# Optimization experiments

Measured on AMD Instinct MI355X. Metric: run time of the kernel, lower is better.

Reference implementation:

```python
import jax, jax.numpy as jnp
import numpy as np

B, T, V, H, L = 2048, 128, 256, 20, 15  # batch, seq_len, vocab, hidden, max_label


def setup_inputs() -> dict:
    key = jax.random.key(0)
    ks = jax.random.split(key, 8)
    g = lambda k, shape, s: (jax.random.normal(k, shape, jnp.float32) * s)
    return {
        "x": jax.random.randint(ks[0], (B, T), 0, V, dtype=jnp.int32),
        "W0": g(ks[1], (V, 3 * H), 0.06),   # input kernel layer 0 [V, 3H] (z|r|h)
        "U0": g(ks[2], (H, 3 * H), 0.2),    # recurrent kernel layer 0
        "b0i": jnp.zeros((3 * H,), jnp.float32),  # input bias (reset_after=True split bias)
        "b0r": jnp.zeros((3 * H,), jnp.float32),  # recurrent bias
        "W1": g(ks[3], (H, 3 * H), 0.2),
        "U1": g(ks[4], (H, 3 * H), 0.2),
        "b1i": jnp.zeros((3 * H,), jnp.float32),
        "b1r": jnp.zeros((3 * H,), jnp.float32),
        "Wd": g(ks[5], (H, L), 0.2),
        "bd": jnp.zeros((L,), jnp.float32),
        "drop_rate": 0,  # identity dropout (deterministic reference)
    }


def _gru_cell(h, xw, U, br):
    # Keras GRUCell with reset_after=True:
    #   xw = x @ W + b_in  (precomputed), rec = h @ U + b_rec
    rec = h @ U + br
    xz, xr, xh = jnp.split(xw, 3, axis=-1)
    rz, rr, rh = jnp.split(rec, 3, axis=-1)
    z = jax.nn.sigmoid(xz + rz)
    r = jax.nn.sigmoid(xr + rr)
    hh = jnp.tanh(xh + r * rh)
    return z * h + (1.0 - z) * hh


def reference(x, W0, U0, b0i, b0r, W1, U1, b1i, b1r, Wd, bd, drop_rate):
    # one_hot(x) @ W0 == gather rows of W0 (same math, no [B,T,V] materialization)
    xW0 = W0[x] + b0i                 # [B, T, 3H]
    xW0 = jnp.swapaxes(xW0, 0, 1)     # [T, B, 3H] for scan over time

    def step(carry, xw_t):
        h0, h1 = carry
        h0 = _gru_cell(h0, xw_t, U0, b0r)
        xw1 = h0 @ W1 + b1i
        h1 = _gru_cell(h1, xw1, U1, b1r)
        return (h0, h1), None

    h0 = jnp.zeros((x.shape[0], H), W0.dtype)
    h1 = jnp.zeros((x.shape[0], H), W0.dtype)
    (h0, h1), _ = jax.lax.scan(step, (h0, h1), xW0)
    # tf.nn.dropout with rate 0 is the identity
    out = h1
    logits = jax.nn.softmax(out @ Wd + bd, axis=-1)  # [B, L]
    return logits
```

## Files before the change

kernel.cpp:

```cpp
#include <hip/hip_runtime.h>


#define BB 2048
#define TT 128
#define HH 20
#define LL 15
#define H3 60

typedef float v2f __attribute__((ext_vector_type(2)));

#if __has_builtin(__builtin_amdgcn_exp2f)
#define EXP2(x) __builtin_amdgcn_exp2f(x)
#else
#define EXP2(x) exp2f(x)
#endif

__device__ __forceinline__ float bclane(float v, int k) {
    return __int_as_float(__builtin_amdgcn_readlane(__float_as_int(v), k));
}
__device__ __forceinline__ float dpp_rshr1(float v) {
    return __int_as_float(__builtin_amdgcn_update_dpp(
        0, __float_as_int(v), 0x111, 0xF, 0xF, true));
}
__device__ __forceinline__ float dpp_rshr2(float v) {
    return __int_as_float(__builtin_amdgcn_update_dpp(
        0, __float_as_int(v), 0x112, 0xF, 0xF, true));
}
__device__ __forceinline__ float fast_rcp(float x) { return __builtin_amdgcn_rcpf(x); }
#define PIN(v) asm volatile("" : "+v"(v))
#define LDSFENCE() asm volatile("" ::: "memory")

extern "C" __global__ __launch_bounds__(256)
__attribute__((amdgpu_waves_per_eu(2, 2)))
void gru2_kernel(const int* __restrict__ x, const float* __restrict__ W0,
                 const float* __restrict__ U0, const float* __restrict__ b0i,
                 const float* __restrict__ b0r, const float* __restrict__ W1,
                 const float* __restrict__ U1, const float* __restrict__ b1i,
                 const float* __restrict__ b1r, const float* __restrict__ Wd,
                 const float* __restrict__ bd, float* __restrict__ out)
{
    const int lane = threadIdx.x & 63;
    const int w = threadIdx.x >> 6;
    const int b = blockIdx.x * 4 + w;
    const int row = lane >> 4;
    const int pos = lane & 15;
    const int pc  = (pos < 15) ? pos : 14;
    const int u   = pc / 3;
    const int p3  = pc % 3;
    const int j   = row * 5 + u;
    const bool home = (pos < 15) && (p3 == 2);
    const int col = p3 * 20 + j;

    const float gsc = (p3 == 2) ? -2.8853900817779268f : -1.4426950408889634f;

    __shared__ __align__(16) float hbuf[4][2][24];
    float* h0buf = &hbuf[w][0][0];
    float* h1buf = &hbuf[w][1][0];
    const float4* h0q = (const float4*)h0buf;
    const float4* h1q = (const float4*)h1buf;
    if (home) { h0buf[j] = 0.f; h1buf[j] = 0.f; }
    LDSFENCE();

    v2f u0p[10], w1p[10], u1p[10];
#pragma unroll
    for (int q = 0; q < 10; ++q) {
        const int k0 = (2 * q) * H3, k1 = (2 * q + 1) * H3;
        u0p[q] = v2f{U0[k0 + col] * gsc, U0[k1 + col] * gsc};
        w1p[q] = v2f{W1[k0 + col] * gsc, W1[k1 + col] * gsc};
        u1p[q] = v2f{U1[k0 + col] * gsc, U1[k1 + col] * gsc};
    }
#pragma unroll
    for (int q = 0; q < 10; ++q) { PIN(u0p[q]); PIN(w1p[q]); PIN(u1p[q]); }
    float bi0 = b0i[col] * gsc, br0 = b0r[col] * gsc;
    float bi1 = b1i[col] * gsc, br1 = b1r[col] * gsc;
    PIN(bi0); PIN(br0); PIN(bi1); PIN(br1);

    const int* xrow = x + b * TT;
    const int tokA = xrow[lane];
    const int tokB = xrow[64 + lane];

    float h0 = 0.f, h1 = 0.f;

    const int tok0 = __builtin_amdgcn_readlane(tokA, 0);
    const int tok1 = __builtin_amdgcn_readlane(tokA, 1);
    int tokn2 = __builtin_amdgcn_readlane(tokA, 2);
    float xw_cur = fmaf(W0[tok0 * H3 + col], gsc, bi0);
    float xw_nxt = W0[tok1 * H3 + col];

    float4 c0[5], c1[5];
    float rec0, xw1, rec1;

#define DOT01()                                                               \
    {                                                                         \
        v2f a0a = v2f{br0, 0.f}, a0b = v2f{0.f, 0.f};                         \
        v2f a1a = v2f{bi1, 0.f}, a1b = v2f{0.f, 0.f};                         \
        _Pragma("unroll")                                                     \
        for (int q = 0; q < 5; ++q) {                                         \
            const v2f hA = v2f{c0[q].x, c0[q].y}, hB = v2f{c0[q].z, c0[q].w}; \
            a0a = __builtin_elementwise_fma(hA, u0p[2 * q], a0a);             \
            a0b = __builtin_elementwise_fma(hB, u0p[2 * q + 1], a0b);         \
            a1a = __builtin_elementwise_fma(hA, w1p[2 * q], a1a);             \
            a1b = __builtin_elementwise_fma(hB, w1p[2 * q + 1], a1b);         \
        }                                                                     \
        { const v2f t = a0a + a0b; rec0 = t.x + t.y; }                        \
        { const v2f t = a1a + a1b; xw1  = t.x + t.y; }                        \
    }
#define DOT2()                                                                \
    {                                                                         \
        v2f a2a = v2f{br1, 0.f}, a2b = v2f{0.f, 0.f};                         \
        _Pragma("unroll")                                                     \
        for (int q = 0; q < 5; ++q) {                                         \
            const v2f gA = v2f{c1[q].x, c1[q].y}, gB = v2f{c1[q].z, c1[q].w}; \
            a2a = __builtin_elementwise_fma(gA, u1p[2 * q], a2a);             \
            a2b = __builtin_elementwise_fma(gB, u1p[2 * q + 1], a2b);         \
        }                                                                     \
        { const v2f t = a2a + a2b; rec1 = t.x + t.y; }                        \
    }
#define GATES(XW, REC, H)                                                     \
    {                                                                         \
        const float e  = EXP2((XW) + (REC));                                  \
        const float t  = fast_rcp(1.f + e);                                   \
        const float rv = dpp_rshr1(t);                                        \
        const float zv = dpp_rshr2(t);                                        \
        const float eh = EXP2(fmaf(rv, (REC), (XW)));                         \
        const float th = fast_rcp(1.f + eh);                                  \
        const float hh = fmaf(2.f, th, -1.f);                                 \
        H = fmaf(zv, (H) - hh, hh);                                           \
    }

    {
        const float pf = W0[tokn2 * H3 + col];
        const int tokn3 = __builtin_amdgcn_readlane(tokA, 3);
        GATES(xw_cur, br0, h0);
        if (home) h0buf[j] = h0;
        LDSFENCE();
#pragma unroll
        for (int q = 0; q < 5; ++q) { c0[q] = h0q[q]; c1[q] = h1q[q]; }
        xw_cur = fmaf(xw_nxt, gsc, bi0); xw_nxt = pf; tokn2 = tokn3;
        DOT01();
    }

#pragma unroll 2
    for (int i = 1; i < TT; ++i) {
        const int t3 = (i + 3 < TT) ? (i + 3) : (TT - 1);
        const float pf = W0[tokn2 * H3 + col];
        const int tokn3 = __builtin_amdgcn_readlane(t3 < 64 ? tokA : tokB, t3 & 63);

        GATES(xw_cur, rec0, h0);
        if (home) h0buf[j] = h0;
        LDSFENCE();
#pragma unroll
        for (int q = 0; q < 5; ++q) c0[q] = h0q[q];

        DOT2();

        GATES(xw1, rec1, h1);
        if (home) h1buf[j] = h1;
        LDSFENCE();
#pragma unroll
        for (int q = 0; q < 5; ++q) c1[q] = h1q[q];

        xw_cur = fmaf(xw_nxt, gsc, bi0); xw_nxt = pf; tokn2 = tokn3;

        DOT01();
    }

    {
        DOT2();
        GATES(xw1, rec1, h1);
        if (home) h1buf[j] = h1;
        LDSFENCE();
    }

    const int l = lane < LL ? lane : LL - 1;
    float acc = bd[l];
#pragma unroll
    for (int k = 0; k < HH; ++k)
        acc = fmaf(h1buf[k], Wd[k * LL + l], acc);

    float m = acc;
#pragma unroll
    for (int i = 0; i < LL; ++i) m = fmaxf(m, bclane(acc, i));
    const float e = __expf(acc - m);
    float s = 0.f;
#pragma unroll
    for (int i = 0; i < LL; ++i) s += bclane(e, i);
    const float pr = e * fast_rcp(s);

    if (lane < LL) out[b * LL + lane] = pr;
}

extern "C" void kernel_launch(void* const* d_in, const int* in_sizes, int n_in,
                              void* d_out, int out_size, void* d_ws, size_t ws_size,
                              hipStream_t stream) {
    const int*   x   = (const int*)  d_in[0];
    const float* W0  = (const float*)d_in[1];
    const float* U0  = (const float*)d_in[2];
    const float* b0i = (const float*)d_in[3];
    const float* b0r = (const float*)d_in[4];
    const float* W1  = (const float*)d_in[5];
    const float* U1  = (const float*)d_in[6];
    const float* b1i = (const float*)d_in[7];
    const float* b1r = (const float*)d_in[8];
    const float* Wd  = (const float*)d_in[9];
    const float* bd  = (const float*)d_in[10];
    float* out = (float*)d_out;

    dim3 grid(BB / 4), block(256);
    hipLaunchKernelGGL(gru2_kernel, grid, block, 0, stream,
                       x, W0, U0, b0i, b0r, W1, U1, b1i, b1r, Wd, bd, out);
}
```

Measured before the change: 121.2 us.

## Process two batch sequences per wave to interleave independent recurrences

Each wave now runs two batch rows at once, interleaving their GRU recurrences so the latency of one chain's gate math, DPP shuffles and LDS round-trips can be hidden behind the other's work. The grid is halved to 256 blocks and the waves-per-EU hint drops from 2 to 1 to leave room for the doubled register state. This trades thread-level parallelism for instruction-level parallelism. With 256 blocks of 4 waves the whole problem is 1024 waves, so it depends on the per-wave ILP hiding latency that occupancy used to cover.

```diff
diff --git a/kernel.cpp b/kernel.cpp
--- a/kernel.cpp
+++ b/kernel.cpp
@@ -31,7 +31,7 @@
 #define LDSFENCE() asm volatile("" ::: "memory")
 
 extern "C" __global__ __launch_bounds__(256)
-__attribute__((amdgpu_waves_per_eu(2, 2)))
+__attribute__((amdgpu_waves_per_eu(1, 1)))
 void gru2_kernel(const int* __restrict__ x, const float* __restrict__ W0,
                  const float* __restrict__ U0, const float* __restrict__ b0i,
                  const float* __restrict__ b0r, const float* __restrict__ W1,
@@ -41,7 +41,6 @@
 {
     const int lane = threadIdx.x & 63;
     const int w = threadIdx.x >> 6;
-    const int b = blockIdx.x * 4 + w;
     const int row = lane >> 4;
     const int pos = lane & 15;
     const int pc  = (pos < 15) ? pos : 14;
@@ -53,12 +52,16 @@
 
     const float gsc = (p3 == 2) ? -2.8853900817779268f : -1.4426950408889634f;
 
-    __shared__ __align__(16) float hbuf[4][2][24];
-    float* h0buf = &hbuf[w][0][0];
-    float* h1buf = &hbuf[w][1][0];
-    const float4* h0q = (const float4*)h0buf;
-    const float4* h1q = (const float4*)h1buf;
-    if (home) { h0buf[j] = 0.f; h1buf[j] = 0.f; }
+    __shared__ __align__(16) float hbuf[4][2][2][24];
+    float* hA0 = &hbuf[w][0][0][0];
+    float* hA1 = &hbuf[w][0][1][0];
+    float* hB0 = &hbuf[w][1][0][0];
+    float* hB1 = &hbuf[w][1][1][0];
+    const float4* qA0 = (const float4*)hA0;
+    const float4* qA1 = (const float4*)hA1;
+    const float4* qB0 = (const float4*)hB0;
+    const float4* qB1 = (const float4*)hB1;
+    if (home) { hA0[j] = 0.f; hA1[j] = 0.f; hB0[j] = 0.f; hB1[j] = 0.f; }
     LDSFENCE();
 
     v2f u0p[10], w1p[10], u1p[10];
@@ -75,119 +78,153 @@
     float bi1 = b1i[col] * gsc, br1 = b1r[col] * gsc;
     PIN(bi0); PIN(br0); PIN(bi1); PIN(br1);
 
-    const int* xrow = x + b * TT;
-    const int tokA = xrow[lane];
-    const int tokB = xrow[64 + lane];
-
-    float h0 = 0.f, h1 = 0.f;
-
-    const int tok0 = __builtin_amdgcn_readlane(tokA, 0);
-    const int tok1 = __builtin_amdgcn_readlane(tokA, 1);
-    int tokn2 = __builtin_amdgcn_readlane(tokA, 2);
-    float xw_cur = fmaf(W0[tok0 * H3 + col], gsc, bi0);
-    float xw_nxt = W0[tok1 * H3 + col];
-
-    float4 c0[5], c1[5];
-    float rec0, xw1, rec1;
-
-#define DOT01()                                                               \
+    const int bA = blockIdx.x * 8 + w * 2;
+    const int* xrA = x + bA * TT;
+    const int* xrB = xrA + TT;
+    const int tAlo = xrA[lane], tAhi = xrA[64 + lane];
+    const int tBlo = xrB[lane], tBhi = xrB[64 + lane];
+
+    float h0A = 0.f, h1A = 0.f, h0B = 0.f, h1B = 0.f;
+
+    int toknA = __builtin_amdgcn_readlane(tAlo, 2);
+    int toknB = __builtin_amdgcn_readlane(tBlo, 2);
+    float xwAc = fmaf(W0[__builtin_amdgcn_readlane(tAlo, 0) * H3 + col], gsc, bi0);
+    float xwAn = W0[__builtin_amdgcn_readlane(tAlo, 1) * H3 + col];
+    float xwBc = fmaf(W0[__builtin_amdgcn_readlane(tBlo, 0) * H3 + col], gsc, bi0);
+    float xwBn = W0[__builtin_amdgcn_readlane(tBlo, 1) * H3 + col];
+
+    float4 cA0[5], cA1[5], cB0[5], cB1[5];
+    float recA0, xwA1, recA1, recB0, xwB1, recB1;
+
+#define DOT01(C, R0, X1)                                                      \
     {                                                                         \
         v2f a0a = v2f{br0, 0.f}, a0b = v2f{0.f, 0.f};                         \
         v2f a1a = v2f{bi1, 0.f}, a1b = v2f{0.f, 0.f};                         \
         _Pragma("unroll")                                                     \
         for (int q = 0; q < 5; ++q) {                                         \
-            const v2f hA = v2f{c0[q].x, c0[q].y}, hB = v2f{c0[q].z, c0[q].w}; \
-            a0a = __builtin_elementwise_fma(hA, u0p[2 * q], a0a);             \
-            a0b = __builtin_elementwise_fma(hB, u0p[2 * q + 1], a0b);         \
-            a1a = __builtin_elementwise_fma(hA, w1p[2 * q], a1a);             \
-            a1b = __builtin_elementwise_fma(hB, w1p[2 * q + 1], a1b);         \
+            const v2f hA_ = v2f{C[q].x, C[q].y}, hB_ = v2f{C[q].z, C[q].w};   \
+            a0a = __builtin_elementwise_fma(hA_, u0p[2 * q], a0a);            \
+            a0b = __builtin_elementwise_fma(hB_, u0p[2 * q + 1], a0b);        \
+            a1a = __builtin_elementwise_fma(hA_, w1p[2 * q], a1a);            \
+            a1b = __builtin_elementwise_fma(hB_, w1p[2 * q + 1], a1b);        \
         }                                                                     \
-        { const v2f t = a0a + a0b; rec0 = t.x + t.y; }                        \
-        { const v2f t = a1a + a1b; xw1  = t.x + t.y; }                        \
-    }
-#define DOT2()                                                                \
+        { const v2f t_ = a0a + a0b; R0 = t_.x + t_.y; }                       \
+        { const v2f t_ = a1a + a1b; X1 = t_.x + t_.y; }                       \
+    }
+#define DOT2(C, R1)                                                           \
     {                                                                         \
         v2f a2a = v2f{br1, 0.f}, a2b = v2f{0.f, 0.f};                         \
         _Pragma("unroll")                                                     \
         for (int q = 0; q < 5; ++q) {                                         \
-            const v2f gA = v2f{c1[q].x, c1[q].y}, gB = v2f{c1[q].z, c1[q].w}; \
-            a2a = __builtin_elementwise_fma(gA, u1p[2 * q], a2a);             \
-            a2b = __builtin_elementwise_fma(gB, u1p[2 * q + 1], a2b);         \
+            const v2f gA_ = v2f{C[q].x, C[q].y}, gB_ = v2f{C[q].z, C[q].w};   \
+            a2a = __builtin_elementwise_fma(gA_, u1p[2 * q], a2a);            \
+            a2b = __builtin_elementwise_fma(gB_, u1p[2 * q + 1], a2b);        \
         }                                                                     \
-        { const v2f t = a2a + a2b; rec1 = t.x + t.y; }                        \
+        { const v2f t_ = a2a + a2b; R1 = t_.x + t_.y; }                       \
     }
 #define GATES(XW, REC, H)                                                     \
     {                                                                         \
-        const float e  = EXP2((XW) + (REC));                                  \
-        const float t  = fast_rcp(1.f + e);                                   \
-        const float rv = dpp_rshr1(t);                                        \
-        const float zv = dpp_rshr2(t);                                        \
-        const float eh = EXP2(fmaf(rv, (REC), (XW)));                         \
-        const float th = fast_rcp(1.f + eh);                                  \
-        const float hh = fmaf(2.f, th, -1.f);                                 \
-        H = fmaf(zv, (H) - hh, hh);                                           \
+        const float e_  = EXP2((XW) + (REC));                                 \
+        const float t_  = fast_rcp(1.f + e_);                                 \
+        const float rv_ = dpp_rshr1(t_);                                      \
+        const float zv_ = dpp_rshr2(t_);                                      \
+        const float eh_ = EXP2(fmaf(rv_, (REC), (XW)));                       \
+        const float th_ = fast_rcp(1.f + eh_);                                \
+        const float hh_ = fmaf(2.f, th_, -1.f);                               \
+        H = fmaf(zv_, (H) - hh_, hh_);                                        \
     }
 
     {
-        const float pf = W0[tokn2 * H3 + col];
-        const int tokn3 = __builtin_amdgcn_readlane(tokA, 3);
-        GATES(xw_cur, br0, h0);
-        if (home) h0buf[j] = h0;
-        LDSFENCE();
-#pragma unroll
-        for (int q = 0; q < 5; ++q) { c0[q] = h0q[q]; c1[q] = h1q[q]; }
-        xw_cur = fmaf(xw_nxt, gsc, bi0); xw_nxt = pf; tokn2 = tokn3;
-        DOT01();
+        const float pfA = W0[toknA * H3 + col];
+        const float pfB = W0[toknB * H3 + col];
+        const int tA3 = __builtin_amdgcn_readlane(tAlo, 3);
+        const int tB3 = __builtin_amdgcn_readlane(tBlo, 3);
+        GATES(xwAc, br0, h0A);
+        GATES(xwBc, br0, h0B);
+        if (home) { hA0[j] = h0A; hB0[j] = h0B; }
+        LDSFENCE();
+#pragma unroll
+        for (int q = 0; q < 5; ++q) {
+            cA0[q] = qA0[q]; cA1[q] = qA1[q];
+            cB0[q] = qB0[q]; cB1[q] = qB1[q];
+        }
+        xwAc = fmaf(xwAn, gsc, bi0); xwAn = pfA; toknA = tA3;
+        xwBc = fmaf(xwBn, gsc, bi0); xwBn = pfB; toknB = tB3;
+        DOT01(cA0, recA0, xwA1);
+        DOT01(cB0, recB0, xwB1);
     }
 
 #pragma unroll 2
     for (int i = 1; i < TT; ++i) {
         const int t3 = (i + 3 < TT) ? (i + 3) : (TT - 1);
-        const float pf = W0[tokn2 * H3 + col];
-        const int tokn3 = __builtin_amdgcn_readlane(t3 < 64 ? tokA : tokB, t3 & 63);
-
-        GATES(xw_cur, rec0, h0);
-        if (home) h0buf[j] = h0;
-        LDSFENCE();
-#pragma unroll
-        for (int q = 0; q < 5; ++q) c0[q] = h0q[q];
-
-        DOT2();
-
-        GATES(xw1, rec1, h1);
-        if (home) h1buf[j] = h1;
-        LDSFENCE();
-#pragma unroll
-        for (int q = 0; q < 5; ++q) c1[q] = h1q[q];
-
-        xw_cur = fmaf(xw_nxt, gsc, bi0); xw_nxt = pf; tokn2 = tokn3;
-
-        DOT01();
+        const float pfA = W0[toknA * H3 + col];
+        const float pfB = W0[toknB * H3 + col];
+        const int tA3 = __builtin_amdgcn_readlane(t3 < 64 ? tAlo : tAhi, t3 & 63);
+        const int tB3 = __builtin_amdgcn_readlane(t3 < 64 ? tBlo : tBhi, t3 & 63);
+
+        GATES(xwAc, recA0, h0A);
+        GATES(xwBc, recB0, h0B);
+        if (home) { hA0[j] = h0A; hB0[j] = h0B; }
+        LDSFENCE();
+#pragma unroll
+        for (int q = 0; q < 5; ++q) { cA0[q] = qA0[q]; cB0[q] = qB0[q]; }
+
+        DOT2(cA1, recA1);
+        DOT2(cB1, recB1);
+
+        GATES(xwA1, recA1, h1A);
+        GATES(xwB1, recB1, h1B);
+        if (home) { hA1[j] = h1A; hB1[j] = h1B; }
+        LDSFENCE();
+#pragma unroll
+        for (int q = 0; q < 5; ++q) { cA1[q] = qA1[q]; cB1[q] = qB1[q]; }
+
+        xwAc = fmaf(xwAn, gsc, bi0); xwAn = pfA; toknA = tA3;
+        xwBc = fmaf(xwBn, gsc, bi0); xwBn = pfB; toknB = tB3;
+
+        DOT01(cA0, recA0, xwA1);
+        DOT01(cB0, recB0, xwB1);
     }
 
     {
-        DOT2();
-        GATES(xw1, rec1, h1);
-        if (home) h1buf[j] = h1;
+        DOT2(cA1, recA1);
+        DOT2(cB1, recB1);
+        GATES(xwA1, recA1, h1A);
+        GATES(xwB1, recB1, h1B);
+        if (home) { hA1[j] = h1A; hB1[j] = h1B; }
         LDSFENCE();
     }
 
     const int l = lane < LL ? lane : LL - 1;
-    float acc = bd[l];
-#pragma unroll
-    for (int k = 0; k < HH; ++k)
-        acc = fmaf(h1buf[k], Wd[k * LL + l], acc);
-
-    float m = acc;
-#pragma unroll
-    for (int i = 0; i < LL; ++i) m = fmaxf(m, bclane(acc, i));
-    const float e = __expf(acc - m);
-    float s = 0.f;
-#pragma unroll
-    for (int i = 0; i < LL; ++i) s += bclane(e, i);
-    const float pr = e * fast_rcp(s);
-
-    if (lane < LL) out[b * LL + lane] = pr;
+    float accA = bd[l], accB = accA;
+#pragma unroll
+    for (int k = 0; k < HH; ++k) {
+        const float wd = Wd[k * LL + l];
+        accA = fmaf(hA1[k], wd, accA);
+        accB = fmaf(hB1[k], wd, accB);
+    }
+
+    float mA = accA, mB = accB;
+#pragma unroll
+    for (int i = 0; i < LL; ++i) {
+        mA = fmaxf(mA, bclane(accA, i));
+        mB = fmaxf(mB, bclane(accB, i));
+    }
+    const float eA = __expf(accA - mA);
+    const float eB = __expf(accB - mB);
+    float sA = 0.f, sB = 0.f;
+#pragma unroll
+    for (int i = 0; i < LL; ++i) {
+        sA += bclane(eA, i);
+        sB += bclane(eB, i);
+    }
+    const float prA = eA * fast_rcp(sA);
+    const float prB = eB * fast_rcp(sB);
+
+    if (lane < LL) {
+        out[bA * LL + lane] = prA;
+        out[(bA + 1) * LL + lane] = prB;
+    }
 }
 
 extern "C" void kernel_launch(void* const* d_in, const int* in_sizes, int n_in,
@@ -206,7 +243,7 @@
     const float* bd  = (const float*)d_in[10];
     float* out = (float*)d_out;
 
-    dim3 grid(BB / 4), block(256);
+    dim3 grid(BB / 8), block(256);
     hipLaunchKernelGGL(gru2_kernel, grid, block, 0, stream,
                        x, W0, U0, b0i, b0r, W1, U1, b1i, b1r, Wd, bd, out);
 }
```

After: 134.1 us. 1.11x slower.

## Split GRU layers across producer/consumer wavefronts with double-buffered LDS

Applied to the files above, without the earlier changes.

Each batch element now uses two wavefronts: one runs layer 0 and the other runs layer 1, one timestep behind, exchanging h0 through a double-buffered shared array. The goal is to overlap the two layers' dependent chains so each wave's serial critical path per step gets shorter. The cost is a block-wide __syncthreads on every step across 8 waves and twice as many threads. The block size doubles to 512 and launch bounds change to match.

```diff
diff --git a/kernel.cpp b/kernel.cpp
--- a/kernel.cpp
+++ b/kernel.cpp
@@ -28,10 +28,8 @@
 }
 __device__ __forceinline__ float fast_rcp(float x) { return __builtin_amdgcn_rcpf(x); }
 #define PIN(v) asm volatile("" : "+v"(v))
-#define LDSFENCE() asm volatile("" ::: "memory")
-
-extern "C" __global__ __launch_bounds__(256)
-__attribute__((amdgpu_waves_per_eu(2, 2)))
+
+extern "C" __global__ __launch_bounds__(512, 4)
 void gru2_kernel(const int* __restrict__ x, const float* __restrict__ W0,
                  const float* __restrict__ U0, const float* __restrict__ b0i,
                  const float* __restrict__ b0r, const float* __restrict__ W1,
@@ -40,8 +38,11 @@
                  const float* __restrict__ bd, float* __restrict__ out)
 {
     const int lane = threadIdx.x & 63;
-    const int w = threadIdx.x >> 6;
-    const int b = blockIdx.x * 4 + w;
+    const int w    = threadIdx.x >> 6;
+    const int g    = w & 3;
+    const int role = w >> 2;
+    const int batch = blockIdx.x * 4 + g;
+
     const int row = lane >> 4;
     const int pos = lane & 15;
     const int pc  = (pos < 15) ? pos : 14;
@@ -53,141 +54,132 @@
 
     const float gsc = (p3 == 2) ? -2.8853900817779268f : -1.4426950408889634f;
 
-    __shared__ __align__(16) float hbuf[4][2][24];
-    float* h0buf = &hbuf[w][0][0];
-    float* h1buf = &hbuf[w][1][0];
-    const float4* h0q = (const float4*)h0buf;
-    const float4* h1q = (const float4*)h1buf;
-    if (home) { h0buf[j] = 0.f; h1buf[j] = 0.f; }
-    LDSFENCE();
-
-    v2f u0p[10], w1p[10], u1p[10];
-#pragma unroll
-    for (int q = 0; q < 10; ++q) {
-        const int k0 = (2 * q) * H3, k1 = (2 * q + 1) * H3;
-        u0p[q] = v2f{U0[k0 + col] * gsc, U0[k1 + col] * gsc};
-        w1p[q] = v2f{W1[k0 + col] * gsc, W1[k1 + col] * gsc};
-        u1p[q] = v2f{U1[k0 + col] * gsc, U1[k1 + col] * gsc};
-    }
-#pragma unroll
-    for (int q = 0; q < 10; ++q) { PIN(u0p[q]); PIN(w1p[q]); PIN(u1p[q]); }
-    float bi0 = b0i[col] * gsc, br0 = b0r[col] * gsc;
-    float bi1 = b1i[col] * gsc, br1 = b1r[col] * gsc;
-    PIN(bi0); PIN(br0); PIN(bi1); PIN(br1);
-
-    const int* xrow = x + b * TT;
-    const int tokA = xrow[lane];
-    const int tokB = xrow[64 + lane];
-
+    __shared__ __align__(16) float h0s[4][2][24];
+    __shared__ __align__(16) float h1s[4][24];
+    float* h0a = &h0s[g][0][0];
+    float* h0b = &h0s[g][1][0];
+    float* h1a = &h1s[g][0];
+    const float4* q0a = (const float4*)h0a;
+    const float4* q0b = (const float4*)h0b;
+    const float4* q1a = (const float4*)h1a;
+
+    v2f wA[10], wB[10];
+    v2f biasP;
+    v2f biasT;
+    float xbias = 0.f;
+    float4 cP[5], cT[5];
     float h0 = 0.f, h1 = 0.f;
 
-    const int tok0 = __builtin_amdgcn_readlane(tokA, 0);
-    const int tok1 = __builtin_amdgcn_readlane(tokA, 1);
-    int tokn2 = __builtin_amdgcn_readlane(tokA, 2);
-    float xw_cur = fmaf(W0[tok0 * H3 + col], gsc, bi0);
-    float xw_nxt = W0[tok1 * H3 + col];
-
-    float4 c0[5], c1[5];
-    float rec0, xw1, rec1;
-
-#define DOT01()                                                               \
+    int tokn2 = 0, tAlo = 0, tAhi = 0;
+    float xw_cur = 0.f, xw_nxt = 0.f;
+
+    if (role == 0) {
+#pragma unroll
+        for (int q = 0; q < 10; ++q) {
+            const int k0 = (2 * q) * H3, k1 = (2 * q + 1) * H3;
+            wA[q] = v2f{U0[k0 + col] * gsc, U0[k1 + col] * gsc};
+        }
+        biasP = v2f{b0r[col] * gsc, 0.f};
+        xbias = b0i[col] * gsc;
+        const int* xrow = x + batch * TT;
+        tAlo = xrow[lane];
+        tAhi = xrow[64 + lane];
+        tokn2  = __builtin_amdgcn_readlane(tAlo, 2);
+        xw_cur = fmaf(W0[__builtin_amdgcn_readlane(tAlo, 0) * H3 + col], gsc, xbias);
+        xw_nxt = W0[__builtin_amdgcn_readlane(tAlo, 1) * H3 + col];
+    } else {
+#pragma unroll
+        for (int q = 0; q < 10; ++q) {
+            const int k0 = (2 * q) * H3, k1 = (2 * q + 1) * H3;
+            wA[q] = v2f{W1[k0 + col] * gsc, W1[k1 + col] * gsc};
+            wB[q] = v2f{U1[k0 + col] * gsc, U1[k1 + col] * gsc};
+        }
+        biasP = v2f{b1r[col] * gsc, 0.f};
+        biasT = v2f{b1i[col] * gsc, 0.f};
+    }
+#pragma unroll
+    for (int q = 0; q < 10; ++q) { PIN(wA[q]); PIN(wB[q]); }
+#pragma unroll
+    for (int q = 0; q < 5; ++q) cP[q] = float4{0.f, 0.f, 0.f, 0.f};
+
+#define DOT1(C, P, BIASV, OUT)                                                \
     {                                                                         \
-        v2f a0a = v2f{br0, 0.f}, a0b = v2f{0.f, 0.f};                         \
-        v2f a1a = v2f{bi1, 0.f}, a1b = v2f{0.f, 0.f};                         \
+        v2f aa = __builtin_elementwise_fma(v2f{C[0].x, C[0].y}, P[0], BIASV); \
+        v2f ab = v2f{C[0].z, C[0].w} * P[1];                                  \
         _Pragma("unroll")                                                     \
-        for (int q = 0; q < 5; ++q) {                                         \
-            const v2f hA = v2f{c0[q].x, c0[q].y}, hB = v2f{c0[q].z, c0[q].w}; \
-            a0a = __builtin_elementwise_fma(hA, u0p[2 * q], a0a);             \
-            a0b = __builtin_elementwise_fma(hB, u0p[2 * q + 1], a0b);         \
-            a1a = __builtin_elementwise_fma(hA, w1p[2 * q], a1a);             \
-            a1b = __builtin_elementwise_fma(hB, w1p[2 * q + 1], a1b);         \
+        for (int q = 1; q < 5; ++q) {                                         \
+            aa = __builtin_elementwise_fma(v2f{C[q].x, C[q].y}, P[2 * q], aa);\
+            ab = __builtin_elementwise_fma(v2f{C[q].z, C[q].w}, P[2 * q + 1], ab);\
         }                                                                     \
-        { const v2f t = a0a + a0b; rec0 = t.x + t.y; }                        \
-        { const v2f t = a1a + a1b; xw1  = t.x + t.y; }                        \
-    }
-#define DOT2()                                                                \
-    {                                                                         \
-        v2f a2a = v2f{br1, 0.f}, a2b = v2f{0.f, 0.f};                         \
-        _Pragma("unroll")                                                     \
-        for (int q = 0; q < 5; ++q) {                                         \
-            const v2f gA = v2f{c1[q].x, c1[q].y}, gB = v2f{c1[q].z, c1[q].w}; \
-            a2a = __builtin_elementwise_fma(gA, u1p[2 * q], a2a);             \
-            a2b = __builtin_elementwise_fma(gB, u1p[2 * q + 1], a2b);         \
-        }                                                                     \
-        { const v2f t = a2a + a2b; rec1 = t.x + t.y; }                        \
+        const v2f t_ = aa + ab;                                               \
+        OUT = t_.x + t_.y;                                                    \
     }
 #define GATES(XW, REC, H)                                                     \
     {                                                                         \
-        const float e  = EXP2((XW) + (REC));                                  \
-        const float t  = fast_rcp(1.f + e);                                   \
-        const float rv = dpp_rshr1(t);                                        \
-        const float zv = dpp_rshr2(t);                                        \
-        const float eh = EXP2(fmaf(rv, (REC), (XW)));                         \
-        const float th = fast_rcp(1.f + eh);                                  \
-        const float hh = fmaf(2.f, th, -1.f);                                 \
-        H = fmaf(zv, (H) - hh, hh);                                           \
-    }
-
-    {
-        const float pf = W0[tokn2 * H3 + col];
-        const int tokn3 = __builtin_amdgcn_readlane(tokA, 3);
-        GATES(xw_cur, br0, h0);
-        if (home) h0buf[j] = h0;
-        LDSFENCE();
-#pragma unroll
-        for (int q = 0; q < 5; ++q) { c0[q] = h0q[q]; c1[q] = h1q[q]; }
-        xw_cur = fmaf(xw_nxt, gsc, bi0); xw_nxt = pf; tokn2 = tokn3;
-        DOT01();
-    }
-
-#pragma unroll 2
-    for (int i = 1; i < TT; ++i) {
-        const int t3 = (i + 3 < TT) ? (i + 3) : (TT - 1);
-        const float pf = W0[tokn2 * H3 + col];
-        const int tokn3 = __builtin_amdgcn_readlane(t3 < 64 ? tokA : tokB, t3 & 63);
-
-        GATES(xw_cur, rec0, h0);
-        if (home) h0buf[j] = h0;
-        LDSFENCE();
-#pragma unroll
-        for (int q = 0; q < 5; ++q) c0[q] = h0q[q];
-
-        DOT2();
-
-        GATES(xw1, rec1, h1);
-        if (home) h1buf[j] = h1;
-        LDSFENCE();
-#pragma unroll
-        for (int q = 0; q < 5; ++q) c1[q] = h1q[q];
-
-        xw_cur = fmaf(xw_nxt, gsc, bi0); xw_nxt = pf; tokn2 = tokn3;
-
-        DOT01();
-    }
-
-    {
-        DOT2();
-        GATES(xw1, rec1, h1);
-        if (home) h1buf[j] = h1;
-        LDSFENCE();
-    }
-
-    const int l = lane < LL ? lane : LL - 1;
-    float acc = bd[l];
-#pragma unroll
-    for (int k = 0; k < HH; ++k)
-        acc = fmaf(h1buf[k], Wd[k * LL + l], acc);
-
-    float m = acc;
-#pragma unroll
-    for (int i = 0; i < LL; ++i) m = fmaxf(m, bclane(acc, i));
-    const float e = __expf(acc - m);
-    float s = 0.f;
-#pragma unroll
-    for (int i = 0; i < LL; ++i) s += bclane(e, i);
-    const float pr = e * fast_rcp(s);
-
-    if (lane < LL) out[b * LL + lane] = pr;
+        const float e_  = EXP2((XW) + (REC));                                 \
+        const float t_  = fast_rcp(1.f + e_);                                 \
+        const float rv_ = dpp_rshr1(t_);                                      \
+        const float zv_ = dpp_rshr2(t_);                                      \
+        const float eh_ = EXP2(fmaf(rv_, (REC), (XW)));                       \
+        const float th_ = fast_rcp(1.f + eh_);                                \
+        const float hh_ = fmaf(2.f, th_, -1.f);                               \
+        H = fmaf(zv_, (H) - hh_, hh_);                                        \
+    }
+
+    for (int t = 0; t <= TT; ++t) {
+        __syncthreads();
+        if (role == 0) {
+            if (t < TT) {
+                const int t3 = (t + 3 < TT) ? (t + 3) : (TT - 1);
+                const float pf = W0[tokn2 * H3 + col];
+                const int tokn3 =
+                    __builtin_amdgcn_readlane(t3 < 64 ? tAlo : tAhi, t3 & 63);
+                float rec0;
+                DOT1(cP, wA, biasP, rec0);
+                GATES(xw_cur, rec0, h0);
+                float* hw = (t & 1) ? h0b : h0a;
+                if (home) hw[j] = h0;
+                const float4* qs = (t & 1) ? q0b : q0a;
+#pragma unroll
+                for (int q = 0; q < 5; ++q) cP[q] = qs[q];
+                xw_cur = fmaf(xw_nxt, gsc, xbias);
+                xw_nxt = pf; tokn2 = tokn3;
+            }
+        } else {
+            if (t > 0) {
+                const float4* qs = ((t - 1) & 1) ? q0b : q0a;
+#pragma unroll
+                for (int q = 0; q < 5; ++q) cT[q] = qs[q];
+                float rec1;
+                DOT1(cP, wB, biasP, rec1);
+                float xw1;
+                DOT1(cT, wA, biasT, xw1);
+                GATES(xw1, rec1, h1);
+                if (home) h1a[j] = h1;
+#pragma unroll
+                for (int q = 0; q < 5; ++q) cP[q] = q1a[q];
+            }
+        }
+    }
+
+    if (role == 1) {
+        const int l = lane < LL ? lane : LL - 1;
+        float acc = bd[l];
+#pragma unroll
+        for (int k = 0; k < HH; ++k)
+            acc = fmaf(h1a[k], Wd[k * LL + l], acc);
+
+        float m = acc;
+#pragma unroll
+        for (int i = 0; i < LL; ++i) m = fmaxf(m, bclane(acc, i));
+        const float e = __expf(acc - m);
+        float s = 0.f;
+#pragma unroll
+        for (int i = 0; i < LL; ++i) s += bclane(e, i);
+        const float pr = e * fast_rcp(s);
+
+        if (lane < LL) out[batch * LL + lane] = pr;
+    }
 }
 
 extern "C" void kernel_launch(void* const* d_in, const int* in_sizes, int n_in,
@@ -206,7 +198,7 @@
     const float* bd  = (const float*)d_in[10];
     float* out = (float*)d_out;
 
-    dim3 grid(BB / 4), block(256);
+    dim3 grid(BB / 4), block(512);
     hipLaunchKernelGGL(gru2_kernel, grid, block, 0, stream,
                        x, W0, U0, b0i, b0r, W1, U1, b1i, b1r, Wd, bd, out);
 }
```

Measured after the change: 137.8 us. +13.7%, slower.
